# Performance work log

Hardware: AMD Instinct MI355X
Metric: run time of the kernel (lower is better)

Reference implementation:

```python
import jax, jax.numpy as jnp
import numpy as np

N = 8192   # supervoxels in current scan (queries: mean_features / ori_coords)
M = 8192   # surrounding supervoxels (keys: sur_sv_feature / sur_sv_coords)
C = 96     # feature channels
OUT = 20   # semantic classes
LG = 2048  # number of labeled supervoxels


def _pairwise_l2(x, y):
    # squared euclidean distances [n, m], clamped at 0 like torch.clamp(d, 0, inf)
    xn = jnp.sum(x * x, axis=1)[:, None]
    yn = jnp.sum(y * y, axis=1)[None, :]
    d = xn + yn - 2.0 * (x @ y.T)
    return jnp.maximum(d, 0.0)


def _cosine_distance(x1, x2, eps=1e-8):
    w1 = jnp.linalg.norm(x1, axis=1, keepdims=True)
    w2 = jnp.linalg.norm(x2, axis=1, keepdims=True)
    return 1.0 - (x1 @ x2.T) / jnp.maximum(w1 * w2.T, eps)


def setup_inputs() -> dict:
    key = jax.random.key(0)
    ks = jax.random.split(key, 8)
    sur_sv_feature = 0.05 * jax.random.normal(ks[0], (M, C), jnp.float32)
    sur_sv_coords = 0.3 * jax.random.normal(ks[1], (M, 3), jnp.float32)
    gt_idx = jax.random.randint(ks[2], (M,), 0, OUT)
    sur_sv_gt = jnp.eye(OUT, dtype=jnp.float32)[gt_idx]
    sv_prob = jax.random.normal(ks[3], (N, OUT), jnp.float32)
    mean_features = 0.05 * jax.random.normal(ks[4], (N, C), jnp.float32)
    ori_coords = 0.3 * jax.random.normal(ks[5], (N, 3), jnp.float32)
    # two near-identity invertible 4x4 pose matrices
    posses = jnp.eye(4, dtype=jnp.float32)[None, :, :] + 0.02 * jax.random.normal(ks[6], (2, 4, 4), jnp.float32)
    ran_mask = jax.random.randint(ks[7], (M,), 0, 20).astype(jnp.int32)  # torch.randint(20, ...)
    return dict(sur_sv_feature=sur_sv_feature, sur_sv_coords=sur_sv_coords,
                sur_sv_gt=sur_sv_gt, sv_prob=sv_prob, mean_features=mean_features,
                ori_coords=ori_coords, posses=posses, ran_mask=ran_mask, lg=LG)


def reference(sur_sv_feature, sur_sv_coords, sur_sv_gt, sv_prob,
              mean_features, ori_coords, posses, ran_mask, lg):
    # branch: rev=1, idx=0, sf=None
    sv_prob_sm = jax.nn.softmax(sv_prob, axis=1)
    ori_coords_in = ori_coords
    # alginment: diff = inv(posses[1]) @ posses[0]; homogeneous transform
    diff = jnp.linalg.inv(posses[1]) @ posses[0]
    homog = jnp.concatenate([sur_sv_coords,
                             jnp.ones((sur_sv_coords.shape[0], 1), sur_sv_coords.dtype)], axis=1)
    al_sur_sv_coords = (homog @ diff.T)[:, :3]

    feat_dist_cos = _cosine_distance(mean_features, sur_sv_feature)          # [N, M]
    coords_dist = _pairwise_l2(ori_coords_in, al_sur_sv_coords) / 0.25       # / 0.5**2
    sim = (1.0 + feat_dist_cos - jnp.exp(-0.5 * coords_dist)).T              # [M, N]
    sm_index = jnp.argmin(sim, axis=1)                                       # [M] nearest query per key

    onehot = sur_sv_gt
    mid_feat = mean_features[sm_index]       # [M, C]
    mid_coord = ori_coords_in[sm_index]      # [M, 3]

    upd = jnp.argmax(onehot, axis=1) < 9
    upd = upd.at[:lg].set(True)
    upd = jnp.logical_or(upd, ran_mask == 1)                                 # random refresh mask

    # masked (instead of gathered) weighted label propagation: zeroed columns
    # contribute nothing to either numerator or denominator -> same math as
    # index-selecting the update columns.
    fd = _pairwise_l2(mean_features, mid_feat)                               # [N, M]
    cd = _pairwise_l2(ori_coords_in, mid_coord) / 0.25
    dist_matric = jnp.exp(-0.5 * cd / 0.25 - 0.5 * fd / 0.09) * upd[None, :].astype(fd.dtype)
    uw = (dist_matric @ onehot) / (jnp.sum(dist_matric, axis=1, keepdims=True) + 1e-16)

    sv_prob_updated = 0.5 * sv_prob_sm + 0.5 * uw

    # re-inject labeled gt where the propagated prob agrees enough
    tmpx = jnp.argmax(onehot[:lg], axis=1)                                   # [lg]
    idx_lg = sm_index[:lg]
    vals = sv_prob_updated[idx_lg, tmpx]
    tmp = vals > 0.1
    tmp = jnp.where(jnp.any(tmp), tmp, vals > 0.0)                           # fallback threshold
    new_rows = jnp.where(tmp[:, None], onehot[:lg], sv_prob_updated[idx_lg])
    sv_prob_updated = sv_prob_updated.at[idx_lg].set(new_rows)

    maxv = jnp.max(sv_prob_updated, axis=1)
    trust9 = maxv >= 0.9
    trust = jnp.where(jnp.any(trust9), trust9, maxv >= 0.85)                 # [N] bool mask (padded form of torch.nonzero)
    pre = jnp.eye(OUT, dtype=sv_prob_updated.dtype)[jnp.argmax(sv_prob_updated, axis=1)]

    m = trust[:, None].astype(mean_features.dtype)
    return (trust, mean_features * m, ori_coords * m, pre * m,
            uw, sv_prob_updated, sm_index)
```

## Files before the change

kernel.cpp:

```cpp
#include <hip/hip_runtime.h>
#include <math.h>

#define N 8192
#define M 8192
#define C 96
#define OUT 20
#define LG 2048

#define KP2 192
#define NSPA 4
#define NSPB 4

typedef _Float16 h8 __attribute__((ext_vector_type(8)));
typedef float    f4 __attribute__((ext_vector_type(4)));

__device__ __forceinline__ void gl_lds16(const h8* g, h8* l) {
    __builtin_amdgcn_global_load_lds(
        (const __attribute__((address_space(1))) unsigned int*)g,
        (__attribute__((address_space(3))) unsigned int*)l,
        16, 0, 0);
}

__device__ __forceinline__ size_t tsm24(int row, int slot) {
    return ((size_t)(row >> 7) * 24 + slot) * 128 + (row & 127);
}

constexpr size_t OFF_DIFF  = 0;
constexpr size_t OFF_AL    = 256;
constexpr size_t OFF_UPDF  = OFF_AL    + (size_t)M*3*4;
constexpr size_t OFF_GTC   = OFF_UPDF  + (size_t)M*4;
constexpr size_t OFF_SMI   = OFF_GTC   + (size_t)M*4;
constexpr size_t OFF_PERM  = OFF_SMI   + (size_t)M*4;
constexpr size_t OFF_AP    = OFF_PERM  + (size_t)M*4;
constexpr size_t OFF_BQ    = OFF_AP    + (size_t)M*KP2*2;
constexpr size_t OFF_MFP   = OFF_BQ    + (size_t)N*KP2*2;
constexpr size_t OFF_MIDH  = OFF_MFP   + (size_t)N*KP2*2;
constexpr size_t OFF_PAV   = OFF_MIDH  + (size_t)(M+256)*192;
constexpr size_t OFF_PAI   = OFF_PAV   + (size_t)NSPA*M*4;
constexpr size_t OFF_PB    = OFF_PAI   + (size_t)NSPA*M*4;
constexpr size_t OFF_VALS  = OFF_PB    + (size_t)NSPB*N*OUT*4;
constexpr size_t OFF_POS   = OFF_VALS  + (size_t)LG*4;
constexpr size_t OFF_MAXV  = OFF_POS   + (size_t)N*4;
constexpr size_t OFF_AMAX  = OFF_MAXV  + (size_t)N*4;
constexpr size_t OFF_FLAGS = OFF_AMAX  + (size_t)N*4;
constexpr size_t OFF_CNT   = OFF_FLAGS + 256;
constexpr size_t OFF_META  = OFF_CNT   + 256;
constexpr size_t OFF_NQ4   = OFF_META  + 256;
constexpr size_t OFF_SIDEQ = OFF_NQ4   + (size_t)N*16;
constexpr size_t OFF_SIDEC = OFF_SIDEQ + (size_t)(M+256)*16;

__global__ void k_diff(const float* __restrict__ posses, float* __restrict__ diff) {
    if (threadIdx.x != 0 || blockIdx.x != 0) return;
    float a[4][8];
    for (int i = 0; i < 4; i++)
        for (int j = 0; j < 4; j++) {
            a[i][j]     = posses[16 + i*4 + j];
            a[i][4 + j] = (i == j) ? 1.f : 0.f;
        }
    for (int col = 0; col < 4; col++) {
        int piv = col; float mx = fabsf(a[col][col]);
        for (int r = col + 1; r < 4; r++) {
            float v = fabsf(a[r][col]);
            if (v > mx) { mx = v; piv = r; }
        }
        if (piv != col)
            for (int j = 0; j < 8; j++) { float t = a[col][j]; a[col][j] = a[piv][j]; a[piv][j] = t; }
        float inv = 1.0f / a[col][col];
        for (int j = 0; j < 8; j++) a[col][j] *= inv;
        for (int r = 0; r < 4; r++) {
            if (r == col) continue;
            float f = a[r][col];
            for (int j = 0; j < 8; j++) a[r][j] -= f * a[col][j];
        }
    }
    for (int i = 0; i < 4; i++)
        for (int j = 0; j < 4; j++) {
            float s = 0.f;
            for (int k = 0; k < 4; k++) s += a[i][4 + k] * posses[k*4 + j];
            diff[i*4 + j] = s;
        }
}

__global__ void k_prep_m(const float* __restrict__ ssf, const float* __restrict__ scoords,
                         const float* __restrict__ gt, const int* __restrict__ ran_mask,
                         const float* __restrict__ diff,
                         float* __restrict__ al, _Float16* __restrict__ aP,
                         float* __restrict__ updf, int* __restrict__ gtcls,
                         int* __restrict__ cnt) {
    __shared__ int hcnt[OUT];
    const int tt = threadIdx.x;
    if (tt < OUT) hcnt[tt] = 0;
    __syncthreads();
    const int m = blockIdx.x * 32 + (tt >> 1);
    const int h = tt & 1;
    {
        const float4* r4 = (const float4*)(ssf + (size_t)m * C);
        float4 row[12]; float s = 0.f;
        #pragma unroll
        for (int c = 0; c < 12; c++) {
            float4 v = r4[h*12 + c];
            row[c] = v;
            s += v.x*v.x + v.y*v.y + v.z*v.z + v.w*v.w;
        }
        s += __shfl_xor(s, 1, 64);
        float scale = 256.0f / sqrtf(s);
        h8* dst = (h8*)aP;
        #pragma unroll
        for (int qq = 0; qq < 6; qq++) {
            int q = h*6 + qq;
            float4 u = row[2*qq], v = row[2*qq+1];
            float xs[8] = {u.x,u.y,u.z,u.w,v.x,v.y,v.z,v.w};
            h8 hi, lo;
            #pragma unroll
            for (int e = 0; e < 8; e++) {
                float xv = xs[e] * scale;
                _Float16 hh = (_Float16)xv;
                hi[e] = hh;
                lo[e] = (_Float16)(xv - (float)hh);
            }
            dst[tsm24(m, q)]      = hi;
            dst[tsm24(m, 12 + q)] = lo;
        }
        if (h == 0) {
            float x = scoords[m*3], y = scoords[m*3+1], z = scoords[m*3+2];
            #pragma unroll
            for (int j = 0; j < 3; j++)
                al[m*3 + j] = diff[j*4+0]*x + diff[j*4+1]*y + diff[j*4+2]*z + diff[j*4+3];
            int best = 0; float bv = gt[(size_t)m*OUT];
            #pragma unroll
            for (int k = 1; k < OUT; k++) {
                float v = gt[(size_t)m*OUT + k];
                if (v > bv) { bv = v; best = k; }
            }
            gtcls[m] = best;
            bool upd = (best < 9 || m < LG || ran_mask[m] == 1);
            updf[m] = upd ? 1.f : 0.f;
            if (upd) atomicAdd(&hcnt[best], 1);
        }
    }
    __syncthreads();
    if (tt < OUT) atomicAdd(&cnt[tt], hcnt[tt]);
}

__global__ void k_prep_n(const float* __restrict__ mf, const float* __restrict__ ori,
                         _Float16* __restrict__ bQ, _Float16* __restrict__ mfP,
                         float4* __restrict__ nq4) {
    const int tt = threadIdx.x;
    const int n = blockIdx.x * 32 + (tt >> 1);
    const int h = tt & 1;
    const float4* r4 = (const float4*)(mf + (size_t)n * C);
    float4 row[12]; float s = 0.f;
    #pragma unroll
    for (int c = 0; c < 12; c++) {
        float4 v = r4[h*12 + c];
        row[c] = v;
        s += v.x*v.x + v.y*v.y + v.z*v.z + v.w*v.w;
    }
    s += __shfl_xor(s, 1, 64);
    if (h == 0) {
        float4 o;
        o.x = ori[n*3]; o.y = ori[n*3+1]; o.z = ori[n*3+2]; o.w = s;
        nq4[n] = o;
    }
    float scn = 256.0f / sqrtf(s);
    h8* dB = (h8*)bQ;
    h8* dF = (h8*)mfP;
    #pragma unroll
    for (int qq = 0; qq < 6; qq++) {
        int q = h*6 + qq;
        float4 u = row[2*qq], v = row[2*qq+1];
        float xs[8] = {u.x,u.y,u.z,u.w,v.x,v.y,v.z,v.w};
        h8 hiN, loN, hiF, loF;
        #pragma unroll
        for (int e = 0; e < 8; e++) {
            float xn = xs[e] * scn;
            _Float16 hn = (_Float16)xn;
            hiN[e] = hn; loN[e] = (_Float16)(xn - (float)hn);
            float xf = xs[e] * 256.0f;
            _Float16 hf = (_Float16)xf;
            hiF[e] = hf; loF[e] = (_Float16)(xf - (float)hf);
        }
        dB[tsm24(n, q)]    = hiN;
        dB[tsm24(n, 12+q)] = loN;
        dF[tsm24(n, q)]    = hiF;
        dF[tsm24(n, 12+q)] = loF;
    }
}

__global__ __launch_bounds__(1024, 1) void k_argmin(
        const _Float16* __restrict__ aP, const _Float16* __restrict__ bQ,
        const float* __restrict__ al, const float4* __restrict__ nq4,
        float* __restrict__ pav, int* __restrict__ pai) {
    __shared__ h8 sA[24*128];
    __shared__ h8 sB[2*24*128];
    __shared__ float xv[4*128];
    __shared__ int   xi[4*128];
    __shared__ float4 sMs[128];
    const int t = threadIdx.x;
    const int wave = t >> 6, lane = t & 63;
    const int col = lane & 15, quad = lane >> 4;
    const int wm = wave >> 2, wn = wave & 3;
    const int m0 = blockIdx.x * 128;
    const int sp = blockIdx.y;

    {
        const h8* gA = (const h8*)aP + (size_t)blockIdx.x * 3072;
        #pragma unroll
        for (int q = 0; q < 3; q++) gl_lds16(gA + q*1024 + t, sA + q*1024 + t);
    }
    if (t < 128) {
        float ax = al[(m0+t)*3+0], ay = al[(m0+t)*3+1], az = al[(m0+t)*3+2];
        sMs[t] = (float4){4.0f*ax, 4.0f*ay, 4.0f*az, -2.0f*(ax*ax+ay*ay+az*az)};
    }
    float best[8]; int bidx[8];
    #pragma unroll
    for (int e = 0; e < 8; e++) { best[e] = 3.4e38f; bidx[e] = 0; }

    const h8* gB = (const h8*)bQ;
    f4 acc[2][4];
    for (int u = 0; u < 32/NSPA; u++) {
        const int tile = sp + u*NSPA;
        __syncthreads();
        {
            const h8* g = gB + (size_t)(2*tile) * 3072;
            #pragma unroll
            for (int q = 0; q < 6; q++) gl_lds16(g + q*1024 + t, sB + q*1024 + t);
        }
        __syncthreads();
        #pragma unroll
        for (int i = 0; i < 2; i++)
            #pragma unroll
            for (int j = 0; j < 4; j++) acc[i][j] = (f4){0.f,0.f,0.f,0.f};

        #pragma unroll
        for (int ks = 0; ks < 3; ks++) {
            const int hs = ks*4 + quad;
            h8 ah[2], alo[2], bh[4], blo[4];
            #pragma unroll
            for (int i = 0; i < 2; i++) {
                int ml = wm*32 + i*16 + col;
                ah[i]  = sA[hs*128 + ml];
                alo[i] = sA[(12+hs)*128 + ml];
            }
            #pragma unroll
            for (int j = 0; j < 4; j++) {
                int r = wn*64 + j*16 + col;
                int tb = (r >> 7) * 3072, rl = r & 127;
                bh[j]  = sB[tb + hs*128 + rl];
                blo[j] = sB[tb + (12+hs)*128 + rl];
            }
            #pragma unroll
            for (int i = 0; i < 2; i++)
                #pragma unroll
                for (int j = 0; j < 4; j++) {
                    acc[i][j] = __builtin_amdgcn_mfma_f32_16x16x32_f16(ah[i],  bh[j],  acc[i][j], 0, 0, 0);
                    acc[i][j] = __builtin_amdgcn_mfma_f32_16x16x32_f16(ah[i],  blo[j], acc[i][j], 0, 0, 0);
                    acc[i][j] = __builtin_amdgcn_mfma_f32_16x16x32_f16(alo[i], bh[j],  acc[i][j], 0, 0, 0);
                }
        }
        const int n0t = tile * 256;
        float4 o4[4]; float bn[4]; int nidx[4];
        #pragma unroll
        for (int j = 0; j < 4; j++) {
            nidx[j] = n0t + wn*64 + j*16 + col;
            o4[j] = nq4[nidx[j]];
            bn[j] = -2.0f*(o4[j].x*o4[j].x + o4[j].y*o4[j].y + o4[j].z*o4[j].z);
        }
        #pragma unroll
        for (int e = 0; e < 8; e++) {
            int ml = wm*32 + (e>>2)*16 + quad*4 + (e&3);
            float4 sm = sMs[ml];
            #pragma unroll
            for (int j = 0; j < 4; j++) {
                float dot = acc[e>>2][j][e&3];
                float c = sm.w + bn[j];
                c = fmaf(sm.z, o4[j].z, c);
                c = fmaf(sm.y, o4[j].y, c);
                c = fmaf(sm.x, o4[j].x, c);
                float sim = fmaf(dot, -(1.0f/65536.0f), 2.0f) - __expf(c);
                if (sim < best[e]) { best[e] = sim; bidx[e] = nidx[j]; }
            }
        }
    }
    #pragma unroll
    for (int e = 0; e < 8; e++) {
        float bv = best[e]; int bi = bidx[e];
        #pragma unroll
        for (int d = 1; d < 16; d <<= 1) {
            float ov = __shfl_xor(bv, d, 64);
            int   oi = __shfl_xor(bi, d, 64);
            if (ov < bv || (ov == bv && oi < bi)) { bv = ov; bi = oi; }
        }
        best[e] = bv; bidx[e] = bi;
    }
    if (col == 0) {
        #pragma unroll
        for (int e = 0; e < 8; e++) {
            int ml = wm*32 + (e>>2)*16 + quad*4 + (e&3);
            xv[wn*128 + ml] = best[e];
            xi[wn*128 + ml] = bidx[e];
        }
    }
    __syncthreads();
    if (t < 128) {
        float bv = xv[t]; int bi = xi[t];
        #pragma unroll
        for (int w = 1; w < 4; w++) {
            float v = xv[w*128 + t]; int i2 = xi[w*128 + t];
            if (v < bv || (v == bv && i2 < bi)) { bv = v; bi = i2; }
        }
        pav[(size_t)sp * M + m0 + t] = bv;
        pai[(size_t)sp * M + m0 + t] = bi;
    }
}

__global__ void k_argmin_reduce(const float* __restrict__ pav, const int* __restrict__ pai,
                                int* __restrict__ smi, float* __restrict__ out_smi) {
    int m = blockIdx.x * 256 + threadIdx.x;
    if (m >= M) return;
    float best = 3.4e38f; int bidx = 0;
    for (int sp = 0; sp < NSPA; sp++) {
        float v = pav[(size_t)sp * M + m];
        int   i = pai[(size_t)sp * M + m];
        if (v < best || (v == best && i < bidx)) { best = v; bidx = i; }
    }
    smi[m] = bidx;
    out_smi[m] = (float)bidx;
}

__global__ void k_scan(const int* __restrict__ cnt, int* __restrict__ meta) {
    if (threadIdx.x != 0 || blockIdx.x != 0) return;
    int run = 0;
    for (int k = 0; k < OUT; k++) { meta[2 + k] = run; run += cnt[k]; }
    meta[0] = run;
    meta[1] = (run + 255) / 256;
}

__global__ void k_permute(const int* __restrict__ gtcls, const float* __restrict__ updf,
                          int* __restrict__ meta, int* __restrict__ perm) {
    int m = blockIdx.x * 256 + threadIdx.x;
    if (m >= M) return;
    if (updf[m] == 0.f) return;
    int pos = atomicAdd(&meta[2 + gtcls[m]], 1);
    perm[pos] = m;
}

__global__ void k_gather_sorted(const int* __restrict__ meta, const int* __restrict__ perm,
                                const int* __restrict__ smi, const int* __restrict__ gtcls,
                                const _Float16* __restrict__ mfP, const float4* __restrict__ nq4,
                                _Float16* __restrict__ midH,
                                float4* __restrict__ sideQ, int* __restrict__ sideC) {
    int tid = blockIdx.x * 256 + threadIdx.x;
    int rr = tid / 12;
    int q  = tid - rr * 12;
    int mact = meta[0];
    int mpad = meta[1] * 256;
    if (rr >= mpad) return;
    h8* dst = (h8*)midH;
    size_t didx = ((size_t)(rr >> 7) * 12 + q) * 128 + (rr & 127);
    if (rr < mact) {
        int m = perm[rr];
        int s = smi[m];
        dst[didx] = ((const h8*)mfP)[tsm24(s, q)];
        if (q == 0) {
            float4 o = nq4[s];
            float4 sq;
            sq.x = o.w;
            sq.y = o.x; sq.z = o.y; sq.w = o.z;
            sideQ[rr] = sq;
            sideC[rr] = gtcls[m];
        }
    } else {
        dst[didx] = (h8)(_Float16)0.f;
        if (q == 0) {
            sideQ[rr] = (float4){1e9f, 0.f, 0.f, 0.f};
            sideC[rr] = 0;
        }
    }
}

__global__ __launch_bounds__(1024, 1) void k_uw(
        const _Float16* __restrict__ mfP, const _Float16* __restrict__ midH,
        const float4* __restrict__ nq4,
        const float4* __restrict__ sideQ, const int* __restrict__ sideC,
        const int* __restrict__ meta, float* __restrict__ pb) {
    __shared__ h8 sN[24*128];
    __shared__ h8 sB[2][2*12*128];
    __shared__ float bins[128*21];
    __shared__ float4 sSa[128];
    __shared__ float  sSb[128];
    const int t = threadIdx.x;
    const int wave = t >> 6, lane = t & 63;
    const int col = lane & 15, quad = lane >> 4;
    const int wm = wave >> 2, wn = wave & 3;
    const int n0 = blockIdx.x * 128;
    const int sp = blockIdx.y;
    const int nmac = meta[1];

    {
        const h8* gN = (const h8*)mfP + (size_t)blockIdx.x * 3072;
        #pragma unroll
        for (int q = 0; q < 3; q++) gl_lds16(gN + q*1024 + t, sN + q*1024 + t);
        if (sp < nmac) {
            const h8* g = (const h8*)midH + (size_t)(2*sp) * 1536;
            #pragma unroll
            for (int q = 0; q < 3; q++) gl_lds16(g + q*1024 + t, sB[0] + q*1024 + t);
        }
    }
    if (t < 128) {
        float4 q = nq4[n0 + t];
        sSa[t] = (float4){q.x, q.y, q.z, -8.0f*(q.x*q.x + q.y*q.y + q.z*q.z)};
        sSb[t] = q.w;
    }
    for (int i = t; i < 128*21; i += 1024) bins[i] = 0.f;

    __syncthreads();

    int cur = 0;
    f4 acc[2][4];
    for (int mt = sp; mt < nmac; mt += NSPB) {
        const int mb = mt * 256;
        if (mt + NSPB < nmac) {
            const h8* g = (const h8*)midH + (size_t)(2*(mt + NSPB)) * 1536;
            #pragma unroll
            for (int q = 0; q < 3; q++) gl_lds16(g + q*1024 + t, sB[cur^1] + q*1024 + t);
        }
        #pragma unroll
        for (int i = 0; i < 2; i++)
            #pragma unroll
            for (int j = 0; j < 4; j++) acc[i][j] = (f4){0.f,0.f,0.f,0.f};

        const h8* sBc = sB[cur];
        #pragma unroll
        for (int ks = 0; ks < 3; ks++) {
            const int hs = ks*4 + quad;
            h8 ah[2], alo[2], bh[4];
            #pragma unroll
            for (int i = 0; i < 2; i++) {
                int ml = wm*32 + i*16 + col;
                ah[i]  = sN[hs*128 + ml];
                alo[i] = sN[(12+hs)*128 + ml];
            }
            #pragma unroll
            for (int j = 0; j < 4; j++) {
                int r = wn*64 + j*16 + col;
                int tb = (r >> 7) * 1536, rl = r & 127;
                bh[j]  = sBc[tb + hs*128 + rl];
            }
            #pragma unroll
            for (int i = 0; i < 2; i++)
                #pragma unroll
                for (int j = 0; j < 4; j++) {
                    acc[i][j] = __builtin_amdgcn_mfma_f32_16x16x32_f16(ah[i],  bh[j], acc[i][j], 0, 0, 0);
                    acc[i][j] = __builtin_amdgcn_mfma_f32_16x16x32_f16(alo[i], bh[j], acc[i][j], 0, 0, 0);
                }
        }
        {
            float m2[4], mx16[4], my16[4], mz16[4], bm[4]; int pc[4];
            #pragma unroll
            for (int j = 0; j < 4; j++) {
                int mm = mb + wn*64 + j*16 + col;
                float4 sq = sideQ[mm];
                m2[j] = sq.x;
                mx16[j] = 16.0f*sq.y; my16[j] = 16.0f*sq.z; mz16[j] = 16.0f*sq.w;
                bm[j] = -8.0f*(sq.y*sq.y + sq.z*sq.z + sq.w*sq.w);
                pc[j] = sideC[mm];
            }
            int seg0 = sideC[mb + wn*64];
            int seg1 = sideC[mb + wn*64 + 63];
            if (seg0 == seg1) {
                #pragma unroll
                for (int e = 0; e < 8; e++) {
                    int nl = wm*32 + (e>>2)*16 + quad*4 + (e&3);
                    float4 sa = sSa[nl];
                    float nn = sSb[nl];
                    float rs = 0.f;
                    #pragma unroll
                    for (int j = 0; j < 4; j++) {
                        float dot = acc[e>>2][j][e&3];
                        float tt = fmaf(dot, -2.0f*(1.0f/65536.0f), nn + m2[j]);
                        float fd = fmaxf(tt, 0.0f);
                        float c = sa.w + bm[j];
                        c = fmaf(sa.z, mz16[j], c);
                        c = fmaf(sa.y, my16[j], c);
                        c = fmaf(sa.x, mx16[j], c);
                        rs += __expf(fmaf(fd, -(0.5f/0.09f), c));
                    }
                    rs += __shfl_xor(rs, 1, 64);
                    rs += __shfl_xor(rs, 2, 64);
                    rs += __shfl_xor(rs, 4, 64);
                    rs += __shfl_xor(rs, 8, 64);
                    if (col == 0) atomicAdd(&bins[nl*21 + seg0], rs);
                }
            } else {
                #pragma unroll
                for (int e = 0; e < 8; e++) {
                    int nl = wm*32 + (e>>2)*16 + quad*4 + (e&3);
                    float4 sa = sSa[nl];
                    float nn = sSb[nl];
                    float w[4];
                    #pragma unroll
                    for (int j = 0; j < 4; j++) {
                        float dot = acc[e>>2][j][e&3];
                        float tt = fmaf(dot, -2.0f*(1.0f/65536.0f), nn + m2[j]);
                        float fd = fmaxf(tt, 0.0f);
                        float c = sa.w + bm[j];
                        c = fmaf(sa.z, mz16[j], c);
                        c = fmaf(sa.y, my16[j], c);
                        c = fmaf(sa.x, mx16[j], c);
                        w[j] = __expf(fmaf(fd, -(0.5f/0.09f), c));
                    }
                    for (int cc = seg0; cc <= seg1; cc++) {
                        float rs = 0.f;
                        #pragma unroll
                        for (int j = 0; j < 4; j++) rs += (pc[j] == cc) ? w[j] : 0.f;
                        rs += __shfl_xor(rs, 1, 64);
                        rs += __shfl_xor(rs, 2, 64);
                        rs += __shfl_xor(rs, 4, 64);
                        rs += __shfl_xor(rs, 8, 64);
                        if (col == 0) atomicAdd(&bins[nl*21 + cc], rs);
                    }
                }
            }
        }
        __syncthreads();
        cur ^= 1;
    }
    __syncthreads();
    for (int i = t; i < 128*OUT; i += 1024) {
        int loc = i / OUT, k = i - loc*OUT;
        pb[((size_t)sp*N + n0 + loc)*OUT + k] = bins[loc*21 + k];
    }
}

__global__ void k_uw_final(const float* __restrict__ pb, const float* __restrict__ svp,
                           float* __restrict__ out_uw, float* __restrict__ out_spu) {
    int n = blockIdx.x * 256 + threadIdx.x;
    if (n >= N) return;
    float s[OUT];
    #pragma unroll
    for (int k = 0; k < OUT; k++) s[k] = 0.f;
    for (int sp = 0; sp < NSPB; sp++) {
        size_t base = ((size_t)sp * N + n) * OUT;
        #pragma unroll
        for (int k = 0; k < OUT; k++) s[k] += pb[base + k];
    }
    float tot = 0.f;
    #pragma unroll
    for (int k = 0; k < OUT; k++) tot += s[k];
    float rden = 1.0f / (tot + 1e-16f);
    float p[OUT]; float mx = -3.4e38f;
    #pragma unroll
    for (int k = 0; k < OUT; k++) { p[k] = svp[(size_t)n*OUT + k]; mx = fmaxf(mx, p[k]); }
    float es = 0.f;
    #pragma unroll
    for (int k = 0; k < OUT; k++) { p[k] = __expf(p[k] - mx); es += p[k]; }
    float res = 1.0f / es;
    #pragma unroll
    for (int k = 0; k < OUT; k++) {
        float uw = s[k] * rden;
        out_uw[(size_t)n*OUT + k] = uw;
        out_spu[(size_t)n*OUT + k] = 0.5f * (p[k] * res) + 0.5f * uw;
    }
}

__global__ void k_scatter_pre(const int* __restrict__ smi, const int* __restrict__ gtcls,
                              const float* __restrict__ spu, float* __restrict__ vals,
                              int* __restrict__ pos, int* __restrict__ flags) {
    int i = blockIdx.x * 256 + threadIdx.x;
    if (i >= LG) return;
    int idx = smi[i];
    float v = spu[(size_t)idx*OUT + gtcls[i]];
    vals[i] = v;
    if (v > 0.1f) atomicOr(&flags[0], 1);
    atomicMax(&pos[idx], i);
}

__global__ void k_scatter_apply(const int* __restrict__ smi, const int* __restrict__ gtcls,
                                const float* __restrict__ vals, const int* __restrict__ pos,
                                const int* __restrict__ flags, float* __restrict__ spu) {
    int i = blockIdx.x * 256 + threadIdx.x;
    if (i >= LG) return;
    int idx = smi[i];
    if (pos[idx] != i) return;
    float v = vals[i];
    bool tmp = flags[0] ? (v > 0.1f) : (v > 0.0f);
    if (!tmp) return;
    int cls = gtcls[i];
    #pragma unroll
    for (int k = 0; k < OUT; k++) spu[(size_t)idx*OUT + k] = (k == cls) ? 1.0f : 0.0f;
}

__global__ void k_trust_pre(const float* __restrict__ spu, float* __restrict__ maxv,
                            int* __restrict__ amax, int* __restrict__ flags) {
    int n = blockIdx.x * 256 + threadIdx.x;
    if (n >= N) return;
    float best = spu[(size_t)n*OUT]; int bi = 0;
    #pragma unroll
    for (int k = 1; k < OUT; k++) {
        float v = spu[(size_t)n*OUT + k];
        if (v > best) { best = v; bi = k; }
    }
    maxv[n] = best; amax[n] = bi;
    if (best >= 0.9f) atomicOr(&flags[1], 1);
}

__global__ void k_finalize(const float* __restrict__ mf, const float* __restrict__ ori,
                           const float* __restrict__ maxv, const int* __restrict__ amax,
                           const int* __restrict__ flags,
                           float* __restrict__ out_trust, float* __restrict__ out_mf,
                           float* __restrict__ out_ori, float* __restrict__ out_pre) {
    int n = blockIdx.x * 256 + threadIdx.x;
    if (n >= N) return;
    float mv = maxv[n];
    bool tr = flags[1] ? (mv >= 0.9f) : (mv >= 0.85f);
    float m = tr ? 1.f : 0.f;
    out_trust[n] = m;
    const float4* src = (const float4*)(mf + (size_t)n * C);
    float4* dst = (float4*)(out_mf + (size_t)n * C);
    #pragma unroll
    for (int c = 0; c < 24; c++) {
        float4 v = src[c];
        v.x *= m; v.y *= m; v.z *= m; v.w *= m;
        dst[c] = v;
    }
    out_ori[n*3]   = ori[n*3]   * m;
    out_ori[n*3+1] = ori[n*3+1] * m;
    out_ori[n*3+2] = ori[n*3+2] * m;
    int bi = amax[n];
    #pragma unroll
    for (int k = 0; k < OUT; k++) out_pre[(size_t)n*OUT + k] = (k == bi) ? m : 0.f;
}

extern "C" void kernel_launch(void* const* d_in, const int* in_sizes, int n_in,
                              void* d_out, int out_size, void* d_ws, size_t ws_size,
                              hipStream_t stream) {
    (void)in_sizes; (void)n_in; (void)out_size; (void)ws_size;
    const float* ssf     = (const float*)d_in[0];
    const float* scoords = (const float*)d_in[1];
    const float* gt      = (const float*)d_in[2];
    const float* svp     = (const float*)d_in[3];
    const float* mf      = (const float*)d_in[4];
    const float* ori     = (const float*)d_in[5];
    const float* posses  = (const float*)d_in[6];
    const int*   ran     = (const int*)d_in[7];

    float* out = (float*)d_out;
    float* out_trust = out;
    float* out_mf    = out_trust + N;
    float* out_ori   = out_mf + (size_t)N*C;
    float* out_pre   = out_ori + (size_t)N*3;
    float* out_uw    = out_pre + (size_t)N*OUT;
    float* out_spu   = out_uw  + (size_t)N*OUT;
    float* out_smi   = out_spu + (size_t)N*OUT;

    char* ws = (char*)d_ws;
    float*     w_diff  = (float*)(ws + OFF_DIFF);
    float*     w_al    = (float*)(ws + OFF_AL);
    float*     w_updf  = (float*)(ws + OFF_UPDF);
    int*       w_gtc   = (int*)(ws + OFF_GTC);
    int*       w_smi   = (int*)(ws + OFF_SMI);
    int*       w_perm  = (int*)(ws + OFF_PERM);
    _Float16*  w_aP    = (_Float16*)(ws + OFF_AP);
    _Float16*  w_bQ    = (_Float16*)(ws + OFF_BQ);
    _Float16*  w_mfP   = (_Float16*)(ws + OFF_MFP);
    _Float16*  w_midH  = (_Float16*)(ws + OFF_MIDH);
    float*     w_pav   = (float*)(ws + OFF_PAV);
    int*       w_pai   = (int*)(ws + OFF_PAI);
    float*     w_pb    = (float*)(ws + OFF_PB);
    float*     w_vals  = (float*)(ws + OFF_VALS);
    int*       w_pos   = (int*)(ws + OFF_POS);
    float*     w_maxv  = (float*)(ws + OFF_MAXV);
    int*       w_amax  = (int*)(ws + OFF_AMAX);
    int*       w_flags = (int*)(ws + OFF_FLAGS);
    int*       w_cnt   = (int*)(ws + OFF_CNT);
    int*       w_meta  = (int*)(ws + OFF_META);
    float4*    w_nq4   = (float4*)(ws + OFF_NQ4);
    float4*    w_sideQ = (float4*)(ws + OFF_SIDEQ);
    int*       w_sideC = (int*)(ws + OFF_SIDEC);

    hipMemsetAsync(w_pos, 0xFF, (size_t)N*4, stream);
    hipMemsetAsync(w_flags, 0, 8, stream);
    hipMemsetAsync(w_cnt, 0, OUT*4, stream);

    k_diff<<<1, 64, 0, stream>>>(posses, w_diff);
    k_prep_m<<<M/32, 64, 0, stream>>>(ssf, scoords, gt, ran, w_diff,
                                      w_al, w_aP, w_updf, w_gtc, w_cnt);
    k_prep_n<<<N/32, 64, 0, stream>>>(mf, ori, w_bQ, w_mfP, w_nq4);
    k_argmin<<<dim3(M/128, NSPA), 1024, 0, stream>>>(w_aP, w_bQ, w_al, w_nq4, w_pav, w_pai);
    k_argmin_reduce<<<M/256, 256, 0, stream>>>(w_pav, w_pai, w_smi, out_smi);
    k_scan<<<1, 64, 0, stream>>>(w_cnt, w_meta);
    k_permute<<<M/256, 256, 0, stream>>>(w_gtc, w_updf, w_meta, w_perm);
    k_gather_sorted<<<((M+256)*12)/256, 256, 0, stream>>>(w_meta, w_perm, w_smi, w_gtc,
                                                          w_mfP, w_nq4,
                                                          w_midH, w_sideQ, w_sideC);
    k_uw<<<dim3(N/128, NSPB), 1024, 0, stream>>>(w_mfP, w_midH, w_nq4,
                                                 w_sideQ, w_sideC, w_meta, w_pb);
    k_uw_final<<<N/256, 256, 0, stream>>>(w_pb, svp, out_uw, out_spu);
    k_scatter_pre<<<LG/256, 256, 0, stream>>>(w_smi, w_gtc, out_spu, w_vals, w_pos, w_flags);
    k_scatter_apply<<<LG/256, 256, 0, stream>>>(w_smi, w_gtc, w_vals, w_pos, w_flags, out_spu);
    k_trust_pre<<<N/256, 256, 0, stream>>>(out_spu, w_maxv, w_amax, w_flags);
    k_finalize<<<N/256, 256, 0, stream>>>(mf, ori, w_maxv, w_amax, w_flags,
                                          out_trust, out_mf, out_ori, out_pre);
}
```

Baseline: 228.3 us.

## Merge small kernels, double-buffer argmin B tiles, switch to exp2f

Fuses k_diff, k_prep_m and k_prep_n into one k_prep launch that computes the pose inverse per block in shared memory, and merges argmin_reduce into k_permute and the two scatter kernels into a single-block k_scatter. The argmin kernel now uses 128-wide B tiles double-buffered with async global-to-LDS loads instead of synchronous 256-wide loads, with smaller per-wave accumulators. Exponentials are rewritten as exp2f with LOG2E folded into the coefficients. The aim is fewer launches and overlapping B loads with MFMA work. The costs are redundant per-block matrix inversion, a narrower N tile per iteration, and serialising the scatter into one block.

New measurement: 235.2 us. +3.0%, slower.

```diff
diff --git a/kernel.cpp b/kernel.cpp
--- a/kernel.cpp
+++ b/kernel.cpp
@@ -10,6 +10,7 @@
 #define KP2 192
 #define NSPA 4
 #define NSPB 4
+#define LOG2E 1.4426950408889634f
 
 typedef _Float16 h8 __attribute__((ext_vector_type(8)));
 typedef float    f4 __attribute__((ext_vector_type(4)));
@@ -25,7 +26,6 @@
     return ((size_t)(row >> 7) * 24 + slot) * 128 + (row & 127);
 }
 
-constexpr size_t OFF_DIFF  = 0;
 constexpr size_t OFF_AL    = 256;
 constexpr size_t OFF_UPDF  = OFF_AL    + (size_t)M*3*4;
 constexpr size_t OFF_GTC   = OFF_UPDF  + (size_t)M*4;
@@ -38,8 +38,7 @@
 constexpr size_t OFF_PAV   = OFF_MIDH  + (size_t)(M+256)*192;
 constexpr size_t OFF_PAI   = OFF_PAV   + (size_t)NSPA*M*4;
 constexpr size_t OFF_PB    = OFF_PAI   + (size_t)NSPA*M*4;
-constexpr size_t OFF_VALS  = OFF_PB    + (size_t)NSPB*N*OUT*4;
-constexpr size_t OFF_POS   = OFF_VALS  + (size_t)LG*4;
+constexpr size_t OFF_POS   = OFF_PB    + (size_t)NSPB*N*OUT*4;
 constexpr size_t OFF_MAXV  = OFF_POS   + (size_t)N*4;
 constexpr size_t OFF_AMAX  = OFF_MAXV  + (size_t)N*4;
 constexpr size_t OFF_FLAGS = OFF_AMAX  + (size_t)N*4;
@@ -49,51 +48,53 @@
 constexpr size_t OFF_SIDEQ = OFF_NQ4   + (size_t)N*16;
 constexpr size_t OFF_SIDEC = OFF_SIDEQ + (size_t)(M+256)*16;
 
-__global__ void k_diff(const float* __restrict__ posses, float* __restrict__ diff) {
-    if (threadIdx.x != 0 || blockIdx.x != 0) return;
-    float a[4][8];
-    for (int i = 0; i < 4; i++)
-        for (int j = 0; j < 4; j++) {
-            a[i][j]     = posses[16 + i*4 + j];
-            a[i][4 + j] = (i == j) ? 1.f : 0.f;
-        }
-    for (int col = 0; col < 4; col++) {
-        int piv = col; float mx = fabsf(a[col][col]);
-        for (int r = col + 1; r < 4; r++) {
-            float v = fabsf(a[r][col]);
-            if (v > mx) { mx = v; piv = r; }
-        }
-        if (piv != col)
-            for (int j = 0; j < 8; j++) { float t = a[col][j]; a[col][j] = a[piv][j]; a[piv][j] = t; }
-        float inv = 1.0f / a[col][col];
-        for (int j = 0; j < 8; j++) a[col][j] *= inv;
-        for (int r = 0; r < 4; r++) {
-            if (r == col) continue;
-            float f = a[r][col];
-            for (int j = 0; j < 8; j++) a[r][j] -= f * a[col][j];
-        }
-    }
-    for (int i = 0; i < 4; i++)
-        for (int j = 0; j < 4; j++) {
-            float s = 0.f;
-            for (int k = 0; k < 4; k++) s += a[i][4 + k] * posses[k*4 + j];
-            diff[i*4 + j] = s;
-        }
-}
-
-__global__ void k_prep_m(const float* __restrict__ ssf, const float* __restrict__ scoords,
-                         const float* __restrict__ gt, const int* __restrict__ ran_mask,
-                         const float* __restrict__ diff,
-                         float* __restrict__ al, _Float16* __restrict__ aP,
-                         float* __restrict__ updf, int* __restrict__ gtcls,
-                         int* __restrict__ cnt) {
-    __shared__ int hcnt[OUT];
+__global__ void k_prep(const float* __restrict__ ssf, const float* __restrict__ scoords,
+                       const float* __restrict__ gt, const int* __restrict__ ran_mask,
+                       const float* __restrict__ posses,
+                       const float* __restrict__ mf, const float* __restrict__ ori,
+                       float* __restrict__ al, _Float16* __restrict__ aP,
+                       float* __restrict__ updf, int* __restrict__ gtcls,
+                       int* __restrict__ cnt,
+                       _Float16* __restrict__ bQ, _Float16* __restrict__ mfP,
+                       float4* __restrict__ nq4) {
     const int tt = threadIdx.x;
-    if (tt < OUT) hcnt[tt] = 0;
-    __syncthreads();
-    const int m = blockIdx.x * 32 + (tt >> 1);
-    const int h = tt & 1;
-    {
+    if (blockIdx.x < 256) {
+        __shared__ int hcnt[OUT];
+        __shared__ float sdiff[12];
+        if (tt == 0) {
+            float a[4][8];
+            for (int i = 0; i < 4; i++)
+                for (int j = 0; j < 4; j++) {
+                    a[i][j]     = posses[16 + i*4 + j];
+                    a[i][4 + j] = (i == j) ? 1.f : 0.f;
+                }
+            for (int col = 0; col < 4; col++) {
+                int piv = col; float mx = fabsf(a[col][col]);
+                for (int r = col + 1; r < 4; r++) {
+                    float v = fabsf(a[r][col]);
+                    if (v > mx) { mx = v; piv = r; }
+                }
+                if (piv != col)
+                    for (int j = 0; j < 8; j++) { float t2 = a[col][j]; a[col][j] = a[piv][j]; a[piv][j] = t2; }
+                float inv = 1.0f / a[col][col];
+                for (int j = 0; j < 8; j++) a[col][j] *= inv;
+                for (int r = 0; r < 4; r++) {
+                    if (r == col) continue;
+                    float f = a[r][col];
+                    for (int j = 0; j < 8; j++) a[r][j] -= f * a[col][j];
+                }
+            }
+            for (int i = 0; i < 3; i++)
+                for (int j = 0; j < 4; j++) {
+                    float s2 = 0.f;
+                    for (int k = 0; k < 4; k++) s2 += a[i][4 + k] * posses[k*4 + j];
+                    sdiff[i*4 + j] = s2;
+                }
+        }
+        if (tt < OUT) hcnt[tt] = 0;
+        __syncthreads();
+        const int m = blockIdx.x * 32 + (tt >> 1);
+        const int h = tt & 1;
         const float4* r4 = (const float4*)(ssf + (size_t)m * C);
         float4 row[12]; float s = 0.f;
         #pragma unroll
@@ -125,7 +126,7 @@
             float x = scoords[m*3], y = scoords[m*3+1], z = scoords[m*3+2];
             #pragma unroll
             for (int j = 0; j < 3; j++)
-                al[m*3 + j] = diff[j*4+0]*x + diff[j*4+1]*y + diff[j*4+2]*z + diff[j*4+3];
+                al[m*3 + j] = sdiff[j*4+0]*x + sdiff[j*4+1]*y + sdiff[j*4+2]*z + sdiff[j*4+3];
             int best = 0; float bv = gt[(size_t)m*OUT];
             #pragma unroll
             for (int k = 1; k < OUT; k++) {
@@ -137,53 +138,48 @@
             updf[m] = upd ? 1.f : 0.f;
             if (upd) atomicAdd(&hcnt[best], 1);
         }
-    }
-    __syncthreads();
-    if (tt < OUT) atomicAdd(&cnt[tt], hcnt[tt]);
-}
-
-__global__ void k_prep_n(const float* __restrict__ mf, const float* __restrict__ ori,
-                         _Float16* __restrict__ bQ, _Float16* __restrict__ mfP,
-                         float4* __restrict__ nq4) {
-    const int tt = threadIdx.x;
-    const int n = blockIdx.x * 32 + (tt >> 1);
-    const int h = tt & 1;
-    const float4* r4 = (const float4*)(mf + (size_t)n * C);
-    float4 row[12]; float s = 0.f;
-    #pragma unroll
-    for (int c = 0; c < 12; c++) {
-        float4 v = r4[h*12 + c];
-        row[c] = v;
-        s += v.x*v.x + v.y*v.y + v.z*v.z + v.w*v.w;
-    }
-    s += __shfl_xor(s, 1, 64);
-    if (h == 0) {
-        float4 o;
-        o.x = ori[n*3]; o.y = ori[n*3+1]; o.z = ori[n*3+2]; o.w = s;
-        nq4[n] = o;
-    }
-    float scn = 256.0f / sqrtf(s);
-    h8* dB = (h8*)bQ;
-    h8* dF = (h8*)mfP;
-    #pragma unroll
-    for (int qq = 0; qq < 6; qq++) {
-        int q = h*6 + qq;
-        float4 u = row[2*qq], v = row[2*qq+1];
-        float xs[8] = {u.x,u.y,u.z,u.w,v.x,v.y,v.z,v.w};
-        h8 hiN, loN, hiF, loF;
-        #pragma unroll
-        for (int e = 0; e < 8; e++) {
-            float xn = xs[e] * scn;
-            _Float16 hn = (_Float16)xn;
-            hiN[e] = hn; loN[e] = (_Float16)(xn - (float)hn);
-            float xf = xs[e] * 256.0f;
-            _Float16 hf = (_Float16)xf;
-            hiF[e] = hf; loF[e] = (_Float16)(xf - (float)hf);
-        }
-        dB[tsm24(n, q)]    = hiN;
-        dB[tsm24(n, 12+q)] = loN;
-        dF[tsm24(n, q)]    = hiF;
-        dF[tsm24(n, 12+q)] = loF;
+        __syncthreads();
+        if (tt < OUT) atomicAdd(&cnt[tt], hcnt[tt]);
+    } else {
+        const int n = (blockIdx.x - 256) * 32 + (tt >> 1);
+        const int h = tt & 1;
+        const float4* r4 = (const float4*)(mf + (size_t)n * C);
+        float4 row[12]; float s = 0.f;
+        #pragma unroll
+        for (int c = 0; c < 12; c++) {
+            float4 v = r4[h*12 + c];
+            row[c] = v;
+            s += v.x*v.x + v.y*v.y + v.z*v.z + v.w*v.w;
+        }
+        s += __shfl_xor(s, 1, 64);
+        if (h == 0) {
+            float4 o;
+            o.x = ori[n*3]; o.y = ori[n*3+1]; o.z = ori[n*3+2]; o.w = s;
+            nq4[n] = o;
+        }
+        float scn = 256.0f / sqrtf(s);
+        h8* dB = (h8*)bQ;
+        h8* dF = (h8*)mfP;
+        #pragma unroll
+        for (int qq = 0; qq < 6; qq++) {
+            int q = h*6 + qq;
+            float4 u = row[2*qq], v = row[2*qq+1];
+            float xs[8] = {u.x,u.y,u.z,u.w,v.x,v.y,v.z,v.w};
+            h8 hiN, loN, hiF, loF;
+            #pragma unroll
+            for (int e = 0; e < 8; e++) {
+                float xn = xs[e] * scn;
+                _Float16 hn = (_Float16)xn;
+                hiN[e] = hn; loN[e] = (_Float16)(xn - (float)hn);
+                float xf = xs[e] * 256.0f;
+                _Float16 hf = (_Float16)xf;
+                hiF[e] = hf; loF[e] = (_Float16)(xf - (float)hf);
+            }
+            dB[tsm24(n, q)]    = hiN;
+            dB[tsm24(n, 12+q)] = loN;
+            dF[tsm24(n, q)]    = hiF;
+            dF[tsm24(n, 12+q)] = loF;
+        }
     }
 }
 
@@ -192,7 +188,7 @@
         const float* __restrict__ al, const float4* __restrict__ nq4,
         float* __restrict__ pav, int* __restrict__ pai) {
     __shared__ h8 sA[24*128];
-    __shared__ h8 sB[2*24*128];
+    __shared__ h8 sB[2][24*128];
     __shared__ float xv[4*128];
     __shared__ int   xi[4*128];
     __shared__ float4 sMs[128];
@@ -207,35 +203,41 @@
         const h8* gA = (const h8*)aP + (size_t)blockIdx.x * 3072;
         #pragma unroll
         for (int q = 0; q < 3; q++) gl_lds16(gA + q*1024 + t, sA + q*1024 + t);
+        const h8* g = (const h8*)bQ + (size_t)sp * 3072;
+        #pragma unroll
+        for (int q = 0; q < 3; q++) gl_lds16(g + q*1024 + t, sB[0] + q*1024 + t);
     }
     if (t < 128) {
         float ax = al[(m0+t)*3+0], ay = al[(m0+t)*3+1], az = al[(m0+t)*3+2];
-        sMs[t] = (float4){4.0f*ax, 4.0f*ay, 4.0f*az, -2.0f*(ax*ax+ay*ay+az*az)};
+        sMs[t] = (float4){4.0f*LOG2E*ax, 4.0f*LOG2E*ay, 4.0f*LOG2E*az,
+                          -2.0f*LOG2E*(ax*ax+ay*ay+az*az)};
     }
     float best[8]; int bidx[8];
     #pragma unroll
     for (int e = 0; e < 8; e++) { best[e] = 3.4e38f; bidx[e] = 0; }
 
-    const h8* gB = (const h8*)bQ;
-    f4 acc[2][4];
-    for (int u = 0; u < 32/NSPA; u++) {
+    __syncthreads();
+
+    const int NT = (N/128) / NSPA;
+    int cur = 0;
+    f4 acc[2][2];
+    for (int u = 0; u < NT; u++) {
         const int tile = sp + u*NSPA;
-        __syncthreads();
-        {
-            const h8* g = gB + (size_t)(2*tile) * 3072;
-            #pragma unroll
-            for (int q = 0; q < 6; q++) gl_lds16(g + q*1024 + t, sB + q*1024 + t);
-        }
-        __syncthreads();
+        if (u + 1 < NT) {
+            const h8* g = (const h8*)bQ + (size_t)(sp + (u+1)*NSPA) * 3072;
+            #pragma unroll
+            for (int q = 0; q < 3; q++) gl_lds16(g + q*1024 + t, sB[cur^1] + q*1024 + t);
+        }
         #pragma unroll
         for (int i = 0; i < 2; i++)
             #pragma unroll
-            for (int j = 0; j < 4; j++) acc[i][j] = (f4){0.f,0.f,0.f,0.f};
-
+            for (int j = 0; j < 2; j++) acc[i][j] = (f4){0.f,0.f,0.f,0.f};
+
+        const h8* sBc = sB[cur];
         #pragma unroll
         for (int ks = 0; ks < 3; ks++) {
             const int hs = ks*4 + quad;
-            h8 ah[2], alo[2], bh[4], blo[4];
+            h8 ah[2], alo[2], bh[2], blo[2];
             #pragma unroll
             for (int i = 0; i < 2; i++) {
                 int ml = wm*32 + i*16 + col;
@@ -243,44 +245,45 @@
                 alo[i] = sA[(12+hs)*128 + ml];
             }
             #pragma unroll
-            for (int j = 0; j < 4; j++) {
-                int r = wn*64 + j*16 + col;
-                int tb = (r >> 7) * 3072, rl = r & 127;
-                bh[j]  = sB[tb + hs*128 + rl];
-                blo[j] = sB[tb + (12+hs)*128 + rl];
+            for (int j = 0; j < 2; j++) {
+                int r = wn*32 + j*16 + col;
+                bh[j]  = sBc[hs*128 + r];
+                blo[j] = sBc[(12+hs)*128 + r];
             }
             #pragma unroll
             for (int i = 0; i < 2; i++)
                 #pragma unroll
-                for (int j = 0; j < 4; j++) {
+                for (int j = 0; j < 2; j++) {
                     acc[i][j] = __builtin_amdgcn_mfma_f32_16x16x32_f16(ah[i],  bh[j],  acc[i][j], 0, 0, 0);
                     acc[i][j] = __builtin_amdgcn_mfma_f32_16x16x32_f16(ah[i],  blo[j], acc[i][j], 0, 0, 0);
                     acc[i][j] = __builtin_amdgcn_mfma_f32_16x16x32_f16(alo[i], bh[j],  acc[i][j], 0, 0, 0);
                 }
         }
-        const int n0t = tile * 256;
-        float4 o4[4]; float bn[4]; int nidx[4];
-        #pragma unroll
-        for (int j = 0; j < 4; j++) {
-            nidx[j] = n0t + wn*64 + j*16 + col;
+        const int n0t = tile * 128;
+        float4 o4[2]; float bn[2]; int nidx[2];
+        #pragma unroll
+        for (int j = 0; j < 2; j++) {
+            nidx[j] = n0t + wn*32 + j*16 + col;
             o4[j] = nq4[nidx[j]];
-            bn[j] = -2.0f*(o4[j].x*o4[j].x + o4[j].y*o4[j].y + o4[j].z*o4[j].z);
+            bn[j] = -2.0f*LOG2E*(o4[j].x*o4[j].x + o4[j].y*o4[j].y + o4[j].z*o4[j].z);
         }
         #pragma unroll
         for (int e = 0; e < 8; e++) {
             int ml = wm*32 + (e>>2)*16 + quad*4 + (e&3);
             float4 sm = sMs[ml];
             #pragma unroll
-            for (int j = 0; j < 4; j++) {
+            for (int j = 0; j < 2; j++) {
                 float dot = acc[e>>2][j][e&3];
                 float c = sm.w + bn[j];
                 c = fmaf(sm.z, o4[j].z, c);
                 c = fmaf(sm.y, o4[j].y, c);
                 c = fmaf(sm.x, o4[j].x, c);
-                float sim = fmaf(dot, -(1.0f/65536.0f), 2.0f) - __expf(c);
+                float sim = fmaf(dot, -(1.0f/65536.0f), 2.0f) - exp2f(c);
                 if (sim < best[e]) { best[e] = sim; bidx[e] = nidx[j]; }
             }
         }
+        __syncthreads();
+        cur ^= 1;
     }
     #pragma unroll
     for (int e = 0; e < 8; e++) {
@@ -314,8 +317,18 @@
     }
 }
 
-__global__ void k_argmin_reduce(const float* __restrict__ pav, const int* __restrict__ pai,
-                                int* __restrict__ smi, float* __restrict__ out_smi) {
+__global__ void k_scan(const int* __restrict__ cnt, int* __restrict__ meta) {
+    if (threadIdx.x != 0 || blockIdx.x != 0) return;
+    int run = 0;
+    for (int k = 0; k < OUT; k++) { meta[2 + k] = run; run += cnt[k]; }
+    meta[0] = run;
+    meta[1] = (run + 255) / 256;
+}
+
+__global__ void k_permute(const float* __restrict__ pav, const int* __restrict__ pai,
+                          const int* __restrict__ gtcls, const float* __restrict__ updf,
+                          int* __restrict__ meta, int* __restrict__ perm,
+                          int* __restrict__ smi, float* __restrict__ out_smi) {
     int m = blockIdx.x * 256 + threadIdx.x;
     if (m >= M) return;
     float best = 3.4e38f; int bidx = 0;
@@ -326,20 +339,6 @@
     }
     smi[m] = bidx;
     out_smi[m] = (float)bidx;
-}
-
-__global__ void k_scan(const int* __restrict__ cnt, int* __restrict__ meta) {
-    if (threadIdx.x != 0 || blockIdx.x != 0) return;
-    int run = 0;
-    for (int k = 0; k < OUT; k++) { meta[2 + k] = run; run += cnt[k]; }
-    meta[0] = run;
-    meta[1] = (run + 255) / 256;
-}
-
-__global__ void k_permute(const int* __restrict__ gtcls, const float* __restrict__ updf,
-                          int* __restrict__ meta, int* __restrict__ perm) {
-    int m = blockIdx.x * 256 + threadIdx.x;
-    if (m >= M) return;
     if (updf[m] == 0.f) return;
     int pos = atomicAdd(&meta[2 + gtcls[m]], 1);
     perm[pos] = m;
@@ -409,7 +408,7 @@
     }
     if (t < 128) {
         float4 q = nq4[n0 + t];
-        sSa[t] = (float4){q.x, q.y, q.z, -8.0f*(q.x*q.x + q.y*q.y + q.z*q.z)};
+        sSa[t] = (float4){q.x, q.y, q.z, -8.0f*LOG2E*(q.x*q.x + q.y*q.y + q.z*q.z)};
         sSb[t] = q.w;
     }
     for (int i = t; i < 128*21; i += 1024) bins[i] = 0.f;
@@ -462,8 +461,8 @@
                 int mm = mb + wn*64 + j*16 + col;
                 float4 sq = sideQ[mm];
                 m2[j] = sq.x;
-                mx16[j] = 16.0f*sq.y; my16[j] = 16.0f*sq.z; mz16[j] = 16.0f*sq.w;
-                bm[j] = -8.0f*(sq.y*sq.y + sq.z*sq.z + sq.w*sq.w);
+                mx16[j] = 16.0f*LOG2E*sq.y; my16[j] = 16.0f*LOG2E*sq.z; mz16[j] = 16.0f*LOG2E*sq.w;
+                bm[j] = -8.0f*LOG2E*(sq.y*sq.y + sq.z*sq.z + sq.w*sq.w);
                 pc[j] = sideC[mm];
             }
             int seg0 = sideC[mb + wn*64];
@@ -484,7 +483,7 @@
                         c = fmaf(sa.z, mz16[j], c);
                         c = fmaf(sa.y, my16[j], c);
                         c = fmaf(sa.x, mx16[j], c);
-                        rs += __expf(fmaf(fd, -(0.5f/0.09f), c));
+                        rs += exp2f(fmaf(fd, -(0.5f/0.09f)*LOG2E, c));
                     }
                     rs += __shfl_xor(rs, 1, 64);
                     rs += __shfl_xor(rs, 2, 64);
@@ -508,7 +507,7 @@
                         c = fmaf(sa.z, mz16[j], c);
                         c = fmaf(sa.y, my16[j], c);
                         c = fmaf(sa.x, mx16[j], c);
-                        w[j] = __expf(fmaf(fd, -(0.5f/0.09f), c));
+                        w[j] = exp2f(fmaf(fd, -(0.5f/0.09f)*LOG2E, c));
                     }
                     for (int cc = seg0; cc <= seg1; cc++) {
                         float rs = 0.f;
@@ -564,31 +563,34 @@
     }
 }
 
-__global__ void k_scatter_pre(const int* __restrict__ smi, const int* __restrict__ gtcls,
-                              const float* __restrict__ spu, float* __restrict__ vals,
-                              int* __restrict__ pos, int* __restrict__ flags) {
-    int i = blockIdx.x * 256 + threadIdx.x;
-    if (i >= LG) return;
-    int idx = smi[i];
-    float v = spu[(size_t)idx*OUT + gtcls[i]];
-    vals[i] = v;
-    if (v > 0.1f) atomicOr(&flags[0], 1);
-    atomicMax(&pos[idx], i);
-}
-
-__global__ void k_scatter_apply(const int* __restrict__ smi, const int* __restrict__ gtcls,
-                                const float* __restrict__ vals, const int* __restrict__ pos,
-                                const int* __restrict__ flags, float* __restrict__ spu) {
-    int i = blockIdx.x * 256 + threadIdx.x;
-    if (i >= LG) return;
-    int idx = smi[i];
-    if (pos[idx] != i) return;
-    float v = vals[i];
-    bool tmp = flags[0] ? (v > 0.1f) : (v > 0.0f);
-    if (!tmp) return;
-    int cls = gtcls[i];
-    #pragma unroll
-    for (int k = 0; k < OUT; k++) spu[(size_t)idx*OUT + k] = (k == cls) ? 1.0f : 0.0f;
+__global__ void k_scatter(const int* __restrict__ smi, const int* __restrict__ gtcls,
+                          float* __restrict__ spu, int* __restrict__ pos) {
+    __shared__ int sflag;
+    const int t = threadIdx.x;
+    if (t == 0) sflag = 0;
+    __syncthreads();
+    float v[2]; int idx[2];
+    #pragma unroll
+    for (int k = 0; k < 2; k++) {
+        int i = t + k*1024;
+        idx[k] = smi[i];
+        v[k] = spu[(size_t)idx[k]*OUT + gtcls[i]];
+        if (v[k] > 0.1f) atomicOr(&sflag, 1);
+        atomicMax(&pos[idx[k]], i);
+    }
+    __syncthreads();
+    const bool any = (sflag != 0);
+    #pragma unroll
+    for (int k = 0; k < 2; k++) {
+        int i = t + k*1024;
+        if (atomicMax(&pos[idx[k]], -1) != i) continue;
+        bool tmp = any ? (v[k] > 0.1f) : (v[k] > 0.0f);
+        if (!tmp) continue;
+        int cls = gtcls[i];
+        #pragma unroll
+        for (int kk = 0; kk < OUT; kk++)
+            spu[(size_t)idx[k]*OUT + kk] = (kk == cls) ? 1.0f : 0.0f;
+    }
 }
 
 __global__ void k_trust_pre(const float* __restrict__ spu, float* __restrict__ maxv,
@@ -655,7 +657,6 @@
     float* out_smi   = out_spu + (size_t)N*OUT;
 
     char* ws = (char*)d_ws;
-    float*     w_diff  = (float*)(ws + OFF_DIFF);
     float*     w_al    = (float*)(ws + OFF_AL);
     float*     w_updf  = (float*)(ws + OFF_UPDF);
     int*       w_gtc   = (int*)(ws + OFF_GTC);
@@ -668,7 +669,6 @@
     float*     w_pav   = (float*)(ws + OFF_PAV);
     int*       w_pai   = (int*)(ws + OFF_PAI);
     float*     w_pb    = (float*)(ws + OFF_PB);
-    float*     w_vals  = (float*)(ws + OFF_VALS);
     int*       w_pos   = (int*)(ws + OFF_POS);
     float*     w_maxv  = (float*)(ws + OFF_MAXV);
     int*       w_amax  = (int*)(ws + OFF_AMAX);
@@ -683,22 +683,20 @@
     hipMemsetAsync(w_flags, 0, 8, stream);
     hipMemsetAsync(w_cnt, 0, OUT*4, stream);
 
-    k_diff<<<1, 64, 0, stream>>>(posses, w_diff);
-    k_prep_m<<<M/32, 64, 0, stream>>>(ssf, scoords, gt, ran, w_diff,
-                                      w_al, w_aP, w_updf, w_gtc, w_cnt);
-    k_prep_n<<<N/32, 64, 0, stream>>>(mf, ori, w_bQ, w_mfP, w_nq4);
+    k_prep<<<512, 64, 0, stream>>>(ssf, scoords, gt, ran, posses, mf, ori,
+                                   w_al, w_aP, w_updf, w_gtc, w_cnt,
+                                   w_bQ, w_mfP, w_nq4);
     k_argmin<<<dim3(M/128, NSPA), 1024, 0, stream>>>(w_aP, w_bQ, w_al, w_nq4, w_pav, w_pai);
-    k_argmin_reduce<<<M/256, 256, 0, stream>>>(w_pav, w_pai, w_smi, out_smi);
     k_scan<<<1, 64, 0, stream>>>(w_cnt, w_meta);
-    k_permute<<<M/256, 256, 0, stream>>>(w_gtc, w_updf, w_meta, w_perm);
+    k_permute<<<M/256, 256, 0, stream>>>(w_pav, w_pai, w_gtc, w_updf, w_meta, w_perm,
+                                         w_smi, out_smi);
     k_gather_sorted<<<((M+256)*12)/256, 256, 0, stream>>>(w_meta, w_perm, w_smi, w_gtc,
                                                           w_mfP, w_nq4,
                                                           w_midH, w_sideQ, w_sideC);
     k_uw<<<dim3(N/128, NSPB), 1024, 0, stream>>>(w_mfP, w_midH, w_nq4,
                                                  w_sideQ, w_sideC, w_meta, w_pb);
     k_uw_final<<<N/256, 256, 0, stream>>>(w_pb, svp, out_uw, out_spu);
-    k_scatter_pre<<<LG/256, 256, 0, stream>>>(w_smi, w_gtc, out_spu, w_vals, w_pos, w_flags);
-    k_scatter_apply<<<LG/256, 256, 0, stream>>>(w_smi, w_gtc, w_vals, w_pos, w_flags, out_spu);
+    k_scatter<<<1, 1024, 0, stream>>>(w_smi, w_gtc, out_spu, w_pos);
     k_trust_pre<<<N/256, 256, 0, stream>>>(out_spu, w_maxv, w_amax, w_flags);
     k_finalize<<<N/256, 256, 0, stream>>>(mf, ori, w_maxv, w_amax, w_flags,
                                           out_trust, out_mf, out_ori, out_pre);
```
